# Optimization experiments

Measured on AMD Instinct MI355X. Metric: run time of the kernel, lower is better.

The kernel has to match this reference:

```python
import jax, jax.numpy as jnp
import numpy as np

B, SQ, SKV, H, NH = 2, 2048, 2048, 1024, 16
HD = H // NH  # head dim = 64


def setup_inputs() -> dict:
    key = jax.random.key(0)
    ks = jax.random.split(key, 10)
    s = 1.0 / np.sqrt(H)
    return {
        "query_states": jax.random.normal(ks[0], (B, SQ, H), jnp.float32),
        "key_value_states": jax.random.normal(ks[1], (B, SKV, H), jnp.float32),
        "attention_mask": jnp.ones((B, SQ, SKV), jnp.float32),
        "Wq": jax.random.normal(ks[2], (H, H), jnp.float32) * s,
        "bq": jnp.zeros((H,), jnp.float32),
        "Wk": jax.random.normal(ks[3], (H, H), jnp.float32) * s,
        "Wv": jax.random.normal(ks[4], (H, H), jnp.float32) * s,
        "bv": jnp.zeros((H,), jnp.float32),
        "Wo": jax.random.normal(ks[5], (H, H), jnp.float32) * s,
        "bo": jnp.zeros((H,), jnp.float32),
    }


def reference(query_states, key_value_states, attention_mask, Wq, bq, Wk, Wv, bv, Wo, bo):
    # projections (torch Linear: x @ W.T + b; key proj has NO bias)
    q = query_states @ Wq.T + bq            # [B,SQ,H]
    k = key_value_states @ Wk.T              # [B,SKV,H]
    v = key_value_states @ Wv.T + bv         # [B,SKV,H]
    # split heads -> [B, NH, S, HD]
    q = q.reshape(B, SQ, NH, HD).transpose(0, 2, 1, 3)
    k = k.reshape(B, SKV, NH, HD).transpose(0, 2, 1, 3)
    v = v.reshape(B, SKV, NH, HD).transpose(0, 2, 1, 3)
    scale = 1.0 / np.sqrt(HD)
    scores = jnp.einsum("bhqd,bhkd->bhqk", q * scale, k)
    # additive mask: (1 - mask) * -10000, broadcast over heads
    scores = scores + ((1.0 - attention_mask) * -10000.0)[:, None, :, :]
    probs = jax.nn.softmax(scores, axis=-1)  # dropout p=0 (eval) -> identity
    ctx = jnp.einsum("bhqk,bhkd->bhqd", probs, v)
    ctx = ctx.transpose(0, 2, 1, 3).reshape(B, SQ, H)
    return ctx @ Wo.T + bo
```

## Files before the change

kernel.cpp:

```cpp
#include <hip/hip_runtime.h>

typedef unsigned short u16;
typedef unsigned int u32;
typedef short s16x8 __attribute__((ext_vector_type(8)));
typedef float f32x4 __attribute__((ext_vector_type(4)));

#define AS1 __attribute__((address_space(1)))
#define AS3 __attribute__((address_space(3)))

#define LOG2E 1.4426950408889634f

__device__ __forceinline__ u16 f2bf(float f) {
  unsigned u = __float_as_uint(f);
  u += 0x7fffu + ((u >> 16) & 1u);
  return (u16)(u >> 16);
}
__device__ __forceinline__ float bf2f(u16 b) {
  return __uint_as_float(((unsigned)b) << 16);
}
__device__ __forceinline__ u32 pack2(float a, float b) {
  return (u32)f2bf(a) | ((u32)f2bf(b) << 16);
}
__device__ __forceinline__ void gld16(const void* g, void* l) {
  __builtin_amdgcn_global_load_lds((const AS1 unsigned int*)g,
                                   (AS3 unsigned int*)l, 16, 0, 0);
}
#define FENCE() asm volatile("" ::: "memory")

__global__ __launch_bounds__(256) void prep_kernel(
    const float* __restrict__ qs, const float* __restrict__ kvs, const float* __restrict__ mk,
    const float* __restrict__ wq, const float* __restrict__ wk, const float* __restrict__ wv,
    const float* __restrict__ wo,
    u16* __restrict__ q_bf, u16* __restrict__ kv_bf, u16* __restrict__ am_bf,
    u16* __restrict__ wq_bf, u16* __restrict__ wk_bf, u16* __restrict__ wv_bf,
    u16* __restrict__ wo_bf)
{
  const int stride = gridDim.x * blockDim.x;
  const float mscale = -10000.f * LOG2E;
  for (int v = blockIdx.x * blockDim.x + threadIdx.x; v < 5242880; v += stride) {
    const float* s; u16* d; int off; bool ismask = false;
    if (v < 1048576)      { s = qs;  d = q_bf;  off = v; }
    else if (v < 2097152) { s = kvs; d = kv_bf; off = v - 1048576; }
    else if (v < 2359296) { s = wq;  d = wq_bf; off = v - 2097152; }
    else if (v < 2621440) { s = wk;  d = wk_bf; off = v - 2359296; }
    else if (v < 2883584) { s = wv;  d = wv_bf; off = v - 2621440; }
    else if (v < 3145728) { s = wo;  d = wo_bf; off = v - 2883584; }
    else                  { s = mk;  d = am_bf; off = v - 3145728; ismask = true; }
    float4 f = ((const float4*)s)[off];
    if (ismask) {
      f.x = (1.f - f.x) * mscale; f.y = (1.f - f.y) * mscale;
      f.z = (1.f - f.z) * mscale; f.w = (1.f - f.w) * mscale;
    }
    ushort4 o;
    o.x = f2bf(f.x); o.y = f2bf(f.y); o.z = f2bf(f.z); o.w = f2bf(f.w);
    ((ushort4*)d)[off] = o;
  }
}

template<int EPI>
__device__ __forceinline__ void gemm_body(
    const u16* __restrict__ A, const u16* __restrict__ W, const float* __restrict__ bias,
    void* __restrict__ outp, float alpha, int m0, int n0)
{
  __shared__ u16 As[3][4096], Bs[3][4096];
  const int tid = threadIdx.x, wave = tid >> 6, lane = tid & 63;
  const int l15 = lane & 15, l4 = lane >> 4;
  const int wr = wave >> 1, wc = wave & 1;

  const int srow = wave * 16 + (lane >> 2);
  const int sslot = ((lane & 3) ^ ((lane >> 3) & 3)) * 8;
  const u16* aS0 = A + (size_t)(m0 + srow) * 1024 + sslot;
  const u16* aS1 = A + (size_t)(m0 + 64 + srow) * 1024 + sslot;
  const u16* bS0 = W + (size_t)(n0 + srow) * 1024 + sslot;
  const u16* bS1 = W + (size_t)(n0 + 64 + srow) * 1024 + sslot;
  const int dOff0 = wave * 512, dOff1 = 2048 + wave * 512;

  const int fswz = ((l15 >> 1) & 3);
  const int afBase = (wr * 64 + l15) * 32 + ((l4 ^ fswz) * 8);
  const int bfBase = (wc * 64 + l15) * 32 + ((l4 ^ fswz) * 8);

  f32x4 acc[4][4] = {};

  auto stage = [&](int buf, int kt) {
    const int ko = kt * 32;
    gld16(aS0 + ko, &As[buf][dOff0]);
    gld16(aS1 + ko, &As[buf][dOff1]);
    gld16(bS0 + ko, &Bs[buf][dOff0]);
    gld16(bS1 + ko, &Bs[buf][dOff1]);
  };

  stage(0, 0);
  stage(1, 1);

  int cb = 0;
  for (int kt = 0; kt < 32; ++kt) {
    if (kt < 31) asm volatile("s_waitcnt vmcnt(4)" ::: "memory");
    else         asm volatile("s_waitcnt vmcnt(0)" ::: "memory");
    __builtin_amdgcn_s_barrier();
    FENCE();
    if (kt < 30) {
      int sb = cb + 2; if (sb >= 3) sb -= 3;
      stage(sb, kt + 2);
    }
    s16x8 af[4], bf[4];
    #pragma unroll
    for (int m = 0; m < 4; ++m) af[m] = *(const s16x8*)&As[cb][afBase + m * 512];
    #pragma unroll
    for (int n = 0; n < 4; ++n) bf[n] = *(const s16x8*)&Bs[cb][bfBase + n * 512];
    __builtin_amdgcn_s_setprio(1);
    #pragma unroll
    for (int m = 0; m < 4; ++m)
      #pragma unroll
      for (int n = 0; n < 4; ++n)
        acc[m][n] = __builtin_amdgcn_mfma_f32_16x16x32_bf16(af[m], bf[n], acc[m][n], 0, 0, 0);
    __builtin_amdgcn_s_setprio(0);
    FENCE();
    cb = (cb + 1 == 3) ? 0 : cb + 1;
  }

  #pragma unroll
  for (int n = 0; n < 4; ++n) {
    const int col = n0 + wc * 64 + n * 16 + l15;
    #pragma unroll
    for (int m = 0; m < 4; ++m) {
      #pragma unroll
      for (int r = 0; r < 4; ++r) {
        const int row = m0 + wr * 64 + m * 16 + l4 * 4 + r;
        if constexpr (EPI == 0) {
          const float val = (acc[m][n][r] + (bias ? bias[col] : 0.f)) * alpha;
          const int bb = row >> 11, ss = row & 2047, hh = col >> 6, dd = col & 63;
          ((u16*)outp)[(((size_t)(bb * 16 + hh)) * 2048 + ss) * 64 + dd] = f2bf(val);
        } else if constexpr (EPI == 1) {
          ((float*)outp)[(size_t)row * 1024 + col] = acc[m][n][r] + (bias ? bias[col] : 0.f);
        } else {
          const float val = acc[m][n][r] + bias[row];
          const int hh = row >> 6, dd = row & 63, bb = col >> 11, ss = col & 2047;
          ((u16*)outp)[(((size_t)(bb * 16 + hh)) * 64 + dd) * 2048 + ss] = f2bf(val);
        }
      }
    }
  }
}

__global__ __launch_bounds__(256) void gemm_qkv(
    const u16* __restrict__ qbf, const u16* __restrict__ kvbf,
    const u16* __restrict__ wqb, const u16* __restrict__ wkb, const u16* __restrict__ wvb,
    const float* __restrict__ bq, const float* __restrict__ bv,
    u16* __restrict__ Qh, u16* __restrict__ Kh, u16* __restrict__ Vt)
{
  const int bid = blockIdx.x;
  const int swz = (bid & 7) * 32 + (bid >> 3);
  const int which = blockIdx.y;
  if (which == 0)
    gemm_body<0>(qbf, wqb, bq, Qh, 0.125f * LOG2E, (swz >> 3) * 128, (swz & 7) * 128);
  else if (which == 1)
    gemm_body<0>(kvbf, wkb, nullptr, Kh, 1.0f, (swz >> 3) * 128, (swz & 7) * 128);
  else
    gemm_body<2>(wvb, kvbf, bv, Vt, 1.0f, (swz >> 5) * 128, (swz & 31) * 128);
}

__global__ __launch_bounds__(256) void gemm_out(
    const u16* __restrict__ ctx, const u16* __restrict__ wob,
    const float* __restrict__ bo, float* __restrict__ out)
{
  const int bid = blockIdx.x;
  const int swz = (bid & 7) * 32 + (bid >> 3);
  gemm_body<1>(ctx, wob, bo, out, 1.0f, (swz >> 3) * 128, (swz & 7) * 128);
}

__global__ __launch_bounds__(256) void attn_kernel(
    const u16* __restrict__ Qh, const u16* __restrict__ Kh,
    const u16* __restrict__ Vt, const u16* __restrict__ am,
    u16* __restrict__ ctx)
{
  __shared__ u16 Ks[3][4096];
  __shared__ u16 Vs[3][4096];
  __shared__ u16 Pl[4][2][1024];
  const int tid = threadIdx.x, wave = tid >> 6, lane = tid & 63;
  const int l15 = lane & 15, l4 = lane >> 4;
  const int x7 = l15 & 7;
  const int bid = blockIdx.x;
  const int pos = (bid & 7) * 64 + (bid >> 3);
  const int hh = pos >> 4, qt = pos & 15;
  const int b = hh >> 4, h = hh & 15;
  const int q0 = qt * 128;
  const u16* Qb = Qh + (size_t)hh * 2048 * 64;
  const u16* Kb = Kh + (size_t)hh * 2048 * 64;
  const u16* Vb = Vt + (size_t)hh * 64 * 2048;

  s16x8 qf[2][2];
  const u16* amrow[2];
  #pragma unroll
  for (int g = 0; g < 2; ++g) {
    const int qrow = q0 + wave * 32 + g * 16 + l15;
    qf[g][0] = *(const s16x8*)(Qb + (size_t)qrow * 64 + l4 * 8);
    qf[g][1] = *(const s16x8*)(Qb + (size_t)qrow * 64 + 32 + l4 * 8);
    amrow[g] = am + ((size_t)b * 2048 + qrow) * 2048;
  }

  const int sr = wave * 16 + (lane >> 3);
  const int ss = ((lane & 7) ^ ((lane >> 3) & 7)) * 8;
  const u16* kS0 = Kb + (size_t)sr * 64 + ss;
  const u16* kS1 = Kb + (size_t)(sr + 8) * 64 + ss;
  const u16* vS0 = Vb + (size_t)sr * 2048 + ss;
  const u16* vS1 = Vb + (size_t)(sr + 8) * 2048 + ss;
  const int kd0 = wave * 1024, kd1 = kd0 + 512;

  auto stage = [&](int buf, int kt) {
    const int kv0 = kt * 64;
    gld16(kS0 + (size_t)kv0 * 64, &Ks[buf][kd0]);
    gld16(kS1 + (size_t)kv0 * 64, &Ks[buf][kd1]);
    gld16(vS0 + kv0, &Vs[buf][kd0]);
    gld16(vS1 + kv0, &Vs[buf][kd1]);
  };

  f32x4 of[2][4] = {};
  float m_run[2] = {-1e30f, -1e30f}, l_run[2] = {0.f, 0.f};
  ushort4 mkC[2][4], mkN[2][4];

  stage(0, 0);
  stage(1, 1);
  #pragma unroll
  for (int g = 0; g < 2; ++g)
    #pragma unroll
    for (int nf = 0; nf < 4; ++nf)
      mkC[g][nf] = *(const ushort4*)(amrow[g] + nf * 16 + l4 * 4);
  asm volatile("s_waitcnt vmcnt(0)" ::: "memory");
  __builtin_amdgcn_s_barrier();
  FENCE();

  int cur = 0;
  for (int kt = 0; kt < 32; ++kt) {
    if (kt < 31) {
      const int kvn = (kt + 1) * 64;
      #pragma unroll
      for (int g = 0; g < 2; ++g)
        #pragma unroll
        for (int nf = 0; nf < 4; ++nf)
          mkN[g][nf] = *(const ushort4*)(amrow[g] + kvn + nf * 16 + l4 * 4);
    }
    if (kt < 30) {
      int sb = cur + 2; if (sb >= 3) sb -= 3;
      stage(sb, kt + 2);
    }

    f32x4 sf[2][4];
    __builtin_amdgcn_s_setprio(1);
    #pragma unroll
    for (int nf = 0; nf < 4; ++nf) {
      const s16x8 ka0 = *(const s16x8*)&Ks[cur][nf * 1024 + l15 * 64 + ((l4 ^ x7) * 8)];
      const s16x8 ka1 = *(const s16x8*)&Ks[cur][nf * 1024 + l15 * 64 + (((4 + l4) ^ x7) * 8)];
      #pragma unroll
      for (int g = 0; g < 2; ++g) {
        f32x4 s = {0.f, 0.f, 0.f, 0.f};
        s = __builtin_amdgcn_mfma_f32_16x16x32_bf16(ka0, qf[g][0], s, 0, 0, 0);
        s = __builtin_amdgcn_mfma_f32_16x16x32_bf16(ka1, qf[g][1], s, 0, 0, 0);
        sf[g][nf] = s;
      }
    }
    __builtin_amdgcn_s_setprio(0);

    #pragma unroll
    for (int g = 0; g < 2; ++g) {
      float tmax = -1e30f;
      #pragma unroll
      for (int nf = 0; nf < 4; ++nf)
        #pragma unroll
        for (int r = 0; r < 4; ++r) {
          const float sv = sf[g][nf][r] + bf2f(((const u16*)&mkC[g][nf])[r]);
          sf[g][nf][r] = sv;
          tmax = fmaxf(tmax, sv);
        }
      tmax = fmaxf(tmax, __shfl_xor(tmax, 16));
      tmax = fmaxf(tmax, __shfl_xor(tmax, 32));

      const float mOld = m_run[g];
      float mn = mOld;
      if (!__all(tmax <= mOld + 11.54f)) {
        mn = fmaxf(mOld, tmax);
        const float sc = exp2f(mOld - mn);
        m_run[g] = mn;
        l_run[g] *= sc;
        float sq[4];
        #pragma unroll
        for (int r = 0; r < 4; ++r) sq[r] = __shfl(sc, l4 * 4 + r);
        #pragma unroll
        for (int nd = 0; nd < 4; ++nd)
          #pragma unroll
          for (int r = 0; r < 4; ++r) of[g][nd][r] *= sq[r];
      }

      float psum = 0.f;
      u32* pw = (u32*)&Pl[wave][g][0];
      #pragma unroll
      for (int nf = 0; nf < 4; ++nf) {
        const float p0 = exp2f(sf[g][nf][0] - mn), p1 = exp2f(sf[g][nf][1] - mn);
        const float p2 = exp2f(sf[g][nf][2] - mn), p3 = exp2f(sf[g][nf][3] - mn);
        psum += (p0 + p1) + (p2 + p3);
        u32* w = pw + l15 * 32 + (((nf * 2 + (l4 >> 1)) ^ x7) * 4) + (l4 & 1) * 2;
        w[0] = pack2(p0, p1);
        w[1] = pack2(p2, p3);
      }
      psum += __shfl_xor(psum, 16);
      psum += __shfl_xor(psum, 32);
      l_run[g] += psum;
    }

    __builtin_amdgcn_s_setprio(1);
    #pragma unroll
    for (int kh = 0; kh < 2; ++kh) {
      s16x8 pa[2];
      #pragma unroll
      for (int g = 0; g < 2; ++g)
        pa[g] = *(const s16x8*)&Pl[wave][g][l15 * 64 + (((kh * 4 + l4) ^ x7) * 8)];
      #pragma unroll
      for (int nd = 0; nd < 4; ++nd) {
        const s16x8 vb = *(const s16x8*)&Vs[cur][nd * 1024 + l15 * 64 + (((kh * 4 + l4) ^ x7) * 8)];
        #pragma unroll
        for (int g = 0; g < 2; ++g)
          of[g][nd] = __builtin_amdgcn_mfma_f32_16x16x32_bf16(pa[g], vb, of[g][nd], 0, 0, 0);
      }
    }
    __builtin_amdgcn_s_setprio(0);

    #pragma unroll
    for (int g = 0; g < 2; ++g)
      #pragma unroll
      for (int nf = 0; nf < 4; ++nf)
        mkC[g][nf] = mkN[g][nf];

    if (kt < 31) {
      asm volatile("s_waitcnt vmcnt(4)" ::: "memory");
      __builtin_amdgcn_s_barrier();
      FENCE();
    }
    cur = (cur + 1 == 3) ? 0 : cur + 1;
  }

  #pragma unroll
  for (int g = 0; g < 2; ++g) {
    const float inv = 1.f / l_run[g];
    float invq[4];
    #pragma unroll
    for (int r = 0; r < 4; ++r) invq[r] = __shfl(inv, l4 * 4 + r);
    #pragma unroll
    for (int r = 0; r < 4; ++r) {
      const int qg = q0 + wave * 32 + g * 16 + l4 * 4 + r;
      const size_t rowbase = ((size_t)b * 2048 + qg) * 1024 + h * 64;
      #pragma unroll
      for (int nd = 0; nd < 4; ++nd)
        ctx[rowbase + nd * 16 + l15] = f2bf(of[g][nd][r] * invq[r]);
    }
  }
}

extern "C" void kernel_launch(void* const* d_in, const int* in_sizes, int n_in,
                              void* d_out, int out_size, void* d_ws, size_t ws_size,
                              hipStream_t stream)
{
  const float* qs = (const float*)d_in[0];
  const float* kvs = (const float*)d_in[1];
  const float* mk = (const float*)d_in[2];
  const float* Wq = (const float*)d_in[3];
  const float* bq = (const float*)d_in[4];
  const float* Wk = (const float*)d_in[5];
  const float* Wv = (const float*)d_in[6];
  const float* bv = (const float*)d_in[7];
  const float* Wo = (const float*)d_in[8];
  const float* bo = (const float*)d_in[9];
  float* out = (float*)d_out;

  char* ws = (char*)d_ws;
  u16* q_bf  = (u16*)(ws + 0);
  u16* kv_bf = (u16*)(ws + 8388608);
  u16* wq_bf = (u16*)(ws + 16777216);
  u16* wk_bf = (u16*)(ws + 18874368);
  u16* wv_bf = (u16*)(ws + 20971520);
  u16* wo_bf = (u16*)(ws + 23068672);
  u16* am_bf = (u16*)(ws + 25165824);
  u16* Qhp   = (u16*)(ws + 41943040);
  u16* Khp   = (u16*)(ws + 50331648);
  u16* Vtp   = (u16*)(ws + 58720256);
  u16* ctxp  = (u16*)(ws + 67108864);

  prep_kernel<<<dim3(2048), dim3(256), 0, stream>>>(
      qs, kvs, mk, Wq, Wk, Wv, Wo, q_bf, kv_bf, am_bf, wq_bf, wk_bf, wv_bf, wo_bf);

  gemm_qkv<<<dim3(256, 3), dim3(256), 0, stream>>>(
      q_bf, kv_bf, wq_bf, wk_bf, wv_bf, bq, bv, Qhp, Khp, Vtp);

  attn_kernel<<<dim3(512), dim3(256), 0, stream>>>(Qhp, Khp, Vtp, am_bf, ctxp);

  gemm_out<<<dim3(256), dim3(256), 0, stream>>>(ctxp, wo_bf, bo, out);
}
```

Measured before the change: 333.3 us.

## Skip all-zero mask tiles in attention, split QKV GEMMs, use hardware bf16 pack

A new flag kernel scans the converted additive mask per 128x64 tile and sets a bit when the tile is all zero. The attention kernel then skips loading and adding the mask for flagged tiles, cutting mask memory traffic. Attention moves from triple to double buffering with a full vmcnt(0) wait each step, which can expose load latency. The fused QKV launch is split into three separate GEMM launches, the s_setprio hints around the GEMM MFMA loop are dropped, and bf16 conversion uses the v_cvt_pk_bf16_f32 instruction. The flag buffer reuses the wq_bf workspace after the Q projection has consumed it.

```diff
diff --git a/kernel.cpp b/kernel.cpp
--- a/kernel.cpp
+++ b/kernel.cpp
@@ -18,14 +18,15 @@
 __device__ __forceinline__ float bf2f(u16 b) {
   return __uint_as_float(((unsigned)b) << 16);
 }
-__device__ __forceinline__ u32 pack2(float a, float b) {
-  return (u32)f2bf(a) | ((u32)f2bf(b) << 16);
+__device__ __forceinline__ u32 cvtpk(float lo, float hi) {
+  u32 r;
+  asm("v_cvt_pk_bf16_f32 %0, %1, %2" : "=v"(r) : "v"(lo), "v"(hi));
+  return r;
 }
 __device__ __forceinline__ void gld16(const void* g, void* l) {
   __builtin_amdgcn_global_load_lds((const AS1 unsigned int*)g,
                                    (AS3 unsigned int*)l, 16, 0, 0);
 }
-#define FENCE() asm volatile("" ::: "memory")
 
 __global__ __launch_bounds__(256) void prep_kernel(
     const float* __restrict__ qs, const float* __restrict__ kvs, const float* __restrict__ mk,
@@ -51,10 +52,31 @@
       f.x = (1.f - f.x) * mscale; f.y = (1.f - f.y) * mscale;
       f.z = (1.f - f.z) * mscale; f.w = (1.f - f.w) * mscale;
     }
-    ushort4 o;
-    o.x = f2bf(f.x); o.y = f2bf(f.y); o.z = f2bf(f.z); o.w = f2bf(f.w);
-    ((ushort4*)d)[off] = o;
-  }
+    uint2 o;
+    o.x = cvtpk(f.x, f.y);
+    o.y = cvtpk(f.z, f.w);
+    ((uint2*)d)[off] = o;
+  }
+}
+
+__global__ __launch_bounds__(256) void flag_kernel(const u16* __restrict__ am,
+                                                   u32* __restrict__ flags)
+{
+  const int fid = blockIdx.x;
+  const int kt = fid & 31, qt = (fid >> 5) & 15, b = fid >> 9;
+  const int t = threadIdx.x;
+  const int row = t >> 1, half = t & 1;
+  const u16* p = am + ((size_t)(b * 2048 + qt * 128 + row)) * 2048 + kt * 64 + half * 32;
+  const uint4 v0 = *(const uint4*)p;
+  const uint4 v1 = *(const uint4*)(p + 16);
+  const u32 acc = v0.x | v0.y | v0.z | v0.w | v1.x | v1.y | v1.z | v1.w;
+  const bool z = (acc & 0x7fff7fffu) == 0;
+  const bool wz = __all(z);
+  __shared__ int ok[4];
+  if ((t & 63) == 0) ok[t >> 6] = wz;
+  __syncthreads();
+  if (t == 0 && ok[0] && ok[1] && ok[2] && ok[3])
+    atomicOr(&flags[(b << 4) + qt], 1u << kt);
 }
 
 template<int EPI>
@@ -97,7 +119,7 @@
     if (kt < 31) asm volatile("s_waitcnt vmcnt(4)" ::: "memory");
     else         asm volatile("s_waitcnt vmcnt(0)" ::: "memory");
     __builtin_amdgcn_s_barrier();
-    FENCE();
+    asm volatile("" ::: "memory");
     if (kt < 30) {
       int sb = cb + 2; if (sb >= 3) sb -= 3;
       stage(sb, kt + 2);
@@ -107,14 +129,12 @@
     for (int m = 0; m < 4; ++m) af[m] = *(const s16x8*)&As[cb][afBase + m * 512];
     #pragma unroll
     for (int n = 0; n < 4; ++n) bf[n] = *(const s16x8*)&Bs[cb][bfBase + n * 512];
-    __builtin_amdgcn_s_setprio(1);
     #pragma unroll
     for (int m = 0; m < 4; ++m)
       #pragma unroll
       for (int n = 0; n < 4; ++n)
         acc[m][n] = __builtin_amdgcn_mfma_f32_16x16x32_bf16(af[m], bf[n], acc[m][n], 0, 0, 0);
-    __builtin_amdgcn_s_setprio(0);
-    FENCE();
+    asm volatile("" ::: "memory");
     cb = (cb + 1 == 3) ? 0 : cb + 1;
   }
 
@@ -142,24 +162,26 @@
   }
 }
 
-__global__ __launch_bounds__(256) void gemm_qkv(
-    const u16* __restrict__ qbf, const u16* __restrict__ kvbf,
-    const u16* __restrict__ wqb, const u16* __restrict__ wkb, const u16* __restrict__ wvb,
-    const float* __restrict__ bq, const float* __restrict__ bv,
-    u16* __restrict__ Qh, u16* __restrict__ Kh, u16* __restrict__ Vt)
+__global__ __launch_bounds__(256) void gemm_nt0(
+    const u16* __restrict__ A, const u16* __restrict__ W, const float* __restrict__ bias,
+    u16* __restrict__ out, float alpha)
 {
   const int bid = blockIdx.x;
   const int swz = (bid & 7) * 32 + (bid >> 3);
-  const int which = blockIdx.y;
-  if (which == 0)
-    gemm_body<0>(qbf, wqb, bq, Qh, 0.125f * LOG2E, (swz >> 3) * 128, (swz & 7) * 128);
-  else if (which == 1)
-    gemm_body<0>(kvbf, wkb, nullptr, Kh, 1.0f, (swz >> 3) * 128, (swz & 7) * 128);
-  else
-    gemm_body<2>(wvb, kvbf, bv, Vt, 1.0f, (swz >> 5) * 128, (swz & 31) * 128);
-}
-
-__global__ __launch_bounds__(256) void gemm_out(
+  gemm_body<0>(A, W, bias, out, alpha, (swz >> 3) * 128, (swz & 7) * 128);
+}
+
+__global__ __launch_bounds__(256) void gemm_vT(
+    const u16* __restrict__ wvb, const u16* __restrict__ kvbf, const float* __restrict__ bv,
+    u16* __restrict__ Vt)
+{
+  const int bid = blockIdx.x;
+  const int m0 = (bid >> 5) * 128;
+  const int n0 = ((bid & 7) + ((bid >> 3) & 3) * 8) * 128;
+  gemm_body<2>(wvb, kvbf, bv, Vt, 1.0f, m0, n0);
+}
+
+__global__ __launch_bounds__(256) void gemm_fin(
     const u16* __restrict__ ctx, const u16* __restrict__ wob,
     const float* __restrict__ bo, float* __restrict__ out)
 {
@@ -171,10 +193,10 @@
 __global__ __launch_bounds__(256) void attn_kernel(
     const u16* __restrict__ Qh, const u16* __restrict__ Kh,
     const u16* __restrict__ Vt, const u16* __restrict__ am,
-    u16* __restrict__ ctx)
-{
-  __shared__ u16 Ks[3][4096];
-  __shared__ u16 Vs[3][4096];
+    const u32* __restrict__ fbitsp, u16* __restrict__ ctx)
+{
+  __shared__ u16 Ks[2][4096];
+  __shared__ u16 Vs[2][4096];
   __shared__ u16 Pl[4][2][1024];
   const int tid = threadIdx.x, wave = tid >> 6, lane = tid & 63;
   const int l15 = lane & 15, l4 = lane >> 4;
@@ -187,6 +209,7 @@
   const u16* Qb = Qh + (size_t)hh * 2048 * 64;
   const u16* Kb = Kh + (size_t)hh * 2048 * 64;
   const u16* Vb = Vt + (size_t)hh * 64 * 2048;
+  const u32 fbits = fbitsp[(b << 4) + qt];
 
   s16x8 qf[2][2];
   const u16* amrow[2];
@@ -216,32 +239,25 @@
 
   f32x4 of[2][4] = {};
   float m_run[2] = {-1e30f, -1e30f}, l_run[2] = {0.f, 0.f};
-  ushort4 mkC[2][4], mkN[2][4];
 
   stage(0, 0);
-  stage(1, 1);
-  #pragma unroll
-  for (int g = 0; g < 2; ++g)
-    #pragma unroll
-    for (int nf = 0; nf < 4; ++nf)
-      mkC[g][nf] = *(const ushort4*)(amrow[g] + nf * 16 + l4 * 4);
   asm volatile("s_waitcnt vmcnt(0)" ::: "memory");
   __builtin_amdgcn_s_barrier();
-  FENCE();
+  asm volatile("" ::: "memory");
 
   int cur = 0;
   for (int kt = 0; kt < 32; ++kt) {
-    if (kt < 31) {
-      const int kvn = (kt + 1) * 64;
+    if (kt < 31) stage(cur ^ 1, kt + 1);
+    const int kv0 = kt * 64;
+    const bool skip = (fbits >> kt) & 1u;
+
+    ushort4 mk4[2][4];
+    if (!skip) {
       #pragma unroll
       for (int g = 0; g < 2; ++g)
         #pragma unroll
         for (int nf = 0; nf < 4; ++nf)
-          mkN[g][nf] = *(const ushort4*)(amrow[g] + kvn + nf * 16 + l4 * 4);
-    }
-    if (kt < 30) {
-      int sb = cur + 2; if (sb >= 3) sb -= 3;
-      stage(sb, kt + 2);
+          mk4[g][nf] = *(const ushort4*)(amrow[g] + kv0 + nf * 16 + l4 * 4);
     }
 
     f32x4 sf[2][4];
@@ -267,7 +283,8 @@
       for (int nf = 0; nf < 4; ++nf)
         #pragma unroll
         for (int r = 0; r < 4; ++r) {
-          const float sv = sf[g][nf][r] + bf2f(((const u16*)&mkC[g][nf])[r]);
+          float sv = sf[g][nf][r];
+          if (!skip) sv += bf2f(((const u16*)&mk4[g][nf])[r]);
           sf[g][nf][r] = sv;
           tmax = fmaxf(tmax, sv);
         }
@@ -298,8 +315,8 @@
         const float p2 = exp2f(sf[g][nf][2] - mn), p3 = exp2f(sf[g][nf][3] - mn);
         psum += (p0 + p1) + (p2 + p3);
         u32* w = pw + l15 * 32 + (((nf * 2 + (l4 >> 1)) ^ x7) * 4) + (l4 & 1) * 2;
-        w[0] = pack2(p0, p1);
-        w[1] = pack2(p2, p3);
+        w[0] = cvtpk(p0, p1);
+        w[1] = cvtpk(p2, p3);
       }
       psum += __shfl_xor(psum, 16);
       psum += __shfl_xor(psum, 32);
@@ -323,18 +340,12 @@
     }
     __builtin_amdgcn_s_setprio(0);
 
-    #pragma unroll
-    for (int g = 0; g < 2; ++g)
-      #pragma unroll
-      for (int nf = 0; nf < 4; ++nf)
-        mkC[g][nf] = mkN[g][nf];
-
     if (kt < 31) {
-      asm volatile("s_waitcnt vmcnt(4)" ::: "memory");
+      asm volatile("s_waitcnt vmcnt(0)" ::: "memory");
       __builtin_amdgcn_s_barrier();
-      FENCE();
-    }
-    cur = (cur + 1 == 3) ? 0 : cur + 1;
+      asm volatile("" ::: "memory");
+    }
+    cur ^= 1;
   }
 
   #pragma unroll
@@ -382,14 +393,19 @@
   u16* Khp   = (u16*)(ws + 50331648);
   u16* Vtp   = (u16*)(ws + 58720256);
   u16* ctxp  = (u16*)(ws + 67108864);
+  u32* flagsp = (u32*)wq_bf;
 
   prep_kernel<<<dim3(2048), dim3(256), 0, stream>>>(
       qs, kvs, mk, Wq, Wk, Wv, Wo, q_bf, kv_bf, am_bf, wq_bf, wk_bf, wv_bf, wo_bf);
 
-  gemm_qkv<<<dim3(256, 3), dim3(256), 0, stream>>>(
-      q_bf, kv_bf, wq_bf, wk_bf, wv_bf, bq, bv, Qhp, Khp, Vtp);
-
-  attn_kernel<<<dim3(512), dim3(256), 0, stream>>>(Qhp, Khp, Vtp, am_bf, ctxp);
-
-  gemm_out<<<dim3(256), dim3(256), 0, stream>>>(ctxp, wo_bf, bo, out);
-}
+  gemm_nt0<<<dim3(256), dim3(256), 0, stream>>>(q_bf, wq_bf, bq, Qhp, 0.125f * LOG2E);
+  gemm_nt0<<<dim3(256), dim3(256), 0, stream>>>(kv_bf, wk_bf, nullptr, Khp, 1.0f);
+  gemm_vT <<<dim3(256), dim3(256), 0, stream>>>(wv_bf, kv_bf, bv, Vtp);
+
+  hipMemsetAsync(flagsp, 0, 128, stream);
+  flag_kernel<<<dim3(1024), dim3(256), 0, stream>>>(am_bf, flagsp);
+
+  attn_kernel<<<dim3(512), dim3(256), 0, stream>>>(Qhp, Khp, Vtp, am_bf, flagsp, ctxp);
+
+  gemm_fin<<<dim3(256), dim3(256), 0, stream>>>(ctxp, wo_bf, bo, out);
+}
```

After: 348.1 us. +4.4%, slower.
